# Kernel optimization log

Hardware: AMD Instinct MI355X
Metric: run time of the kernel (lower is better)

Reference implementation:

```python
import jax, jax.numpy as jnp
import numpy as np

N_EMBD = 1024
N_HEAD = 16
HEAD_DIM = N_EMBD // N_HEAD


def setup_inputs() -> dict:
    key = jax.random.key(0)
    ks = jax.random.split(key, 5)
    scale = 0.02
    x = jax.random.normal(ks[0], (2, 2048, N_EMBD), dtype=jnp.float32)
    w_attn = jax.random.normal(ks[1], (N_EMBD, 3 * N_EMBD), dtype=jnp.float32) * scale
    b_attn = jax.random.normal(ks[2], (3 * N_EMBD,), dtype=jnp.float32) * scale
    w_proj = jax.random.normal(ks[3], (N_EMBD, N_EMBD), dtype=jnp.float32) * scale
    b_proj = jax.random.normal(ks[4], (N_EMBD,), dtype=jnp.float32) * scale
    return {"x": x, "w_attn": w_attn, "b_attn": b_attn, "w_proj": w_proj, "b_proj": b_proj}


def reference(x, w_attn, b_attn, w_proj, b_proj):
    B, T, C = x.shape
    qkv = x @ w_attn + b_attn  # [B,T,3C]
    q, k, v = jnp.split(qkv, 3, axis=-1)
    # [B, H, T, D]
    q = q.reshape(B, T, N_HEAD, HEAD_DIM).transpose(0, 2, 1, 3)
    k = k.reshape(B, T, N_HEAD, HEAD_DIM).transpose(0, 2, 1, 3)
    v = v.reshape(B, T, N_HEAD, HEAD_DIM).transpose(0, 2, 1, 3)
    att = jnp.einsum("bhqd,bhkd->bhqk", q, k) * (1.0 / np.sqrt(HEAD_DIM))
    causal = jnp.tril(jnp.ones((T, T), dtype=bool))
    att = jnp.where(causal[None, None], att, jnp.float32(-jnp.inf))
    att = jax.nn.softmax(att, axis=-1)
    y = jnp.einsum("bhqk,bhkd->bhqd", att, v)  # [B,H,T,D]
    y = y.transpose(0, 2, 1, 3).reshape(B, T, C)
    return y @ w_proj + b_proj
```

## Files before the change

### kernel.cpp

```cpp
#include <hip/hip_runtime.h>
#include <stdint.h>

#define SEQ   2048
#define EMBD  1024
#define M_ROWS 4096

typedef unsigned short u16;
typedef unsigned int u32;
typedef __attribute__((ext_vector_type(8))) short bf16x8;
typedef __attribute__((ext_vector_type(4))) float f32x4;

__device__ __forceinline__ u16 f2b(float f) {
  u32 x = __float_as_uint(f);
  return (u16)((x + 0x7FFFu + ((x >> 16) & 1u)) >> 16);
}

__device__ __forceinline__ u32 pkbf(float a, float b) {
  u32 r;
  asm("v_cvt_pk_bf16_f32 %0, %1, %2" : "=v"(r) : "v"(a), "v"(b));
  return r;
}

__device__ __forceinline__ float exp2fast(float x) {
#if __has_builtin(__builtin_amdgcn_exp2f)
  return __builtin_amdgcn_exp2f(x);
#else
  return __expf(x * 0.69314718f);
#endif
}

__device__ __forceinline__ float rcpfast(float x) {
#if __has_builtin(__builtin_amdgcn_rcpf)
  return __builtin_amdgcn_rcpf(x);
#else
  return 1.f / x;
#endif
}

#define AS1(p) ((const __attribute__((address_space(1))) void*)(uintptr_t)(p))
#define AS3(p) ((__attribute__((address_space(3))) void*)(uintptr_t)(p))

__global__ __launch_bounds__(256) void prep(
    const float* __restrict__ x, u16* __restrict__ xb,
    const float* __restrict__ wa, u16* __restrict__ wat,
    const float* __restrict__ wp, u16* __restrict__ wpt) {
  __shared__ float t[64][65];
  const int bx = blockIdx.x;
  if (bx < 1024) {
    const size_t idx = (size_t)bx * 256 + threadIdx.x;
    const float4* p = (const float4*)x + 4 * idx;
    uint4 o0, o1;
    {
      float4 a = p[0], b = p[1];
      o0.x = (u32)f2b(a.x) | ((u32)f2b(a.y) << 16);
      o0.y = (u32)f2b(a.z) | ((u32)f2b(a.w) << 16);
      o0.z = (u32)f2b(b.x) | ((u32)f2b(b.y) << 16);
      o0.w = (u32)f2b(b.z) | ((u32)f2b(b.w) << 16);
    }
    {
      float4 a = p[2], b = p[3];
      o1.x = (u32)f2b(a.x) | ((u32)f2b(a.y) << 16);
      o1.y = (u32)f2b(a.z) | ((u32)f2b(a.w) << 16);
      o1.z = (u32)f2b(b.x) | ((u32)f2b(b.y) << 16);
      o1.w = (u32)f2b(b.z) | ((u32)f2b(b.w) << 16);
    }
    ((uint4*)xb)[2 * idx] = o0;
    ((uint4*)xb)[2 * idx + 1] = o1;
    return;
  }
  const int tt = bx - 1024;
  const int bxr = tt & 63, by = tt >> 6;
  const float* w = (bxr < 48) ? wa : wp;
  u16* wt = (bxr < 48) ? wat : wpt;
  const int N = (bxr < 48) ? 3072 : 1024;
  const int bxt = (bxr < 48) ? bxr : bxr - 48;
  const int K = 1024;
  const int n0 = bxt * 64, k0 = by * 64;
  const int c = threadIdx.x & 63, r4 = threadIdx.x >> 6;
#pragma unroll
  for (int j = 0; j < 16; ++j) {
    const int r = j * 4 + r4;
    t[c][r] = w[(size_t)(k0 + r) * N + n0 + c];
  }
  __syncthreads();
#pragma unroll
  for (int j = 0; j < 16; ++j) {
    const int nr = j * 4 + r4;
    wt[(size_t)(n0 + nr) * K + k0 + c] = f2b(t[nr][c]);
  }
}

template <bool OUT_BF16>
__global__ __launch_bounds__(256) void gemm_kmajor(
    const u16* __restrict__ A, const u16* __restrict__ Bt,
    const float* __restrict__ bias, void* __restrict__ outp,
    int M, int N, int K, int nbx) {
  __shared__ __align__(16) u16 sm[2][2][128 * 32];

  const int nwg = gridDim.x;
  const int qq = nwg >> 3, rr = nwg & 7;
  const int xcd = blockIdx.x & 7, off = blockIdx.x >> 3;
  const int wgid = (xcd < rr ? xcd * (qq + 1) : rr * (qq + 1) + (xcd - rr) * qq) + off;
  const int bx = wgid % nbx, by = wgid / nbx;
  const int row0 = by * 128, col0 = bx * 128;

  const int tid = threadIdx.x;
  const int w = tid >> 6, lane = tid & 63;
  const int wrow = (w >> 1) * 64, wcol = (w & 1) * 64;

  f32x4 acc[4][4];
#pragma unroll
  for (int a = 0; a < 4; ++a)
#pragma unroll
    for (int b = 0; b < 4; ++b)
#pragma unroll
      for (int e = 0; e < 4; ++e) acc[a][b][e] = 0.f;

  const size_t Kb = (size_t)K * 2;

  auto stage = [&](int k0, int buf) {
#pragma unroll
    for (int c = 0; c < 4; ++c) {
      const int ch = w * 4 + c;
      const int i = ch & 7;
      const int rloc = i * 16 + (lane >> 2);
      const int kb = ((lane & 3) * 16) ^ ((rloc & 3) << 4);
      const u16* mat = (ch < 8) ? A : Bt;
      const int r0 = (ch < 8) ? row0 : col0;
      const char* src = (const char*)mat + (size_t)(r0 + rloc) * Kb + k0 * 2 + kb;
      char* dst = (char*)&sm[buf][(ch < 8) ? 0 : 1][0] + i * 1024;
      __builtin_amdgcn_global_load_lds(AS1(src), AS3(dst), 16, 0, 0);
    }
  };

  auto compute = [&](int buf) {
    bf16x8 af[4], bfr[4];
    const char* As = (const char*)&sm[buf][0][0];
    const char* Bs = (const char*)&sm[buf][1][0];
#pragma unroll
    for (int rb = 0; rb < 4; ++rb) {
      const int rl = wrow + rb * 16 + (lane & 15);
      const int kb2 = ((lane >> 4) * 16) ^ ((rl & 3) << 4);
      af[rb] = *(const bf16x8*)(As + rl * 64 + kb2);
    }
#pragma unroll
    for (int cb = 0; cb < 4; ++cb) {
      const int rl = wcol + cb * 16 + (lane & 15);
      const int kb2 = ((lane >> 4) * 16) ^ ((rl & 3) << 4);
      bfr[cb] = *(const bf16x8*)(Bs + rl * 64 + kb2);
    }
#pragma unroll
    for (int rb = 0; rb < 4; ++rb)
#pragma unroll
      for (int cb = 0; cb < 4; ++cb)
        acc[rb][cb] = __builtin_amdgcn_mfma_f32_16x16x32_bf16(
            af[rb], bfr[cb], acc[rb][cb], 0, 0, 0);
  };

  const int nt = K >> 5;
  stage(0, 0);
  int cur = 0;
  for (int t = 0; t < nt - 1; ++t) {
    __syncthreads();
    stage((t + 1) * 32, cur ^ 1);
    compute(cur);
    cur ^= 1;
  }
  __syncthreads();
  compute(cur);

#pragma unroll
  for (int cb = 0; cb < 4; ++cb) {
    const int colg = col0 + wcol + cb * 16 + (lane & 15);
    const float bv = bias[colg];
#pragma unroll
    for (int rb = 0; rb < 4; ++rb) {
#pragma unroll
      for (int i = 0; i < 4; ++i) {
        const int rowg = row0 + wrow + rb * 16 + (lane >> 4) * 4 + i;
        const float v = acc[rb][cb][i] + bv;
        if (OUT_BF16) {
          const u32 hv = f2b(v);
          const u32 pv = (u32)__shfl_xor((int)hv, 1);
          if (!(lane & 1))
            *(u32*)((u16*)outp + (size_t)rowg * N + colg) = hv | (pv << 16);
        } else {
          ((float*)outp)[(size_t)rowg * N + colg] = v;
        }
      }
    }
  }
}

__global__ __launch_bounds__(256, 4) void attn_mfma2(
    const u16* __restrict__ qkvb, u16* __restrict__ yb) {
  __shared__ __align__(16) char lds[32768];

  const int bx = blockIdx.x;
  const int xcd = bx & 7, g = bx >> 3;
  const int j = g >> 5, r = g & 31;
  const int bh = xcd * 4 + j;
  const int qt = (j & 1) ? r : 31 - r;
  const int bb = bh >> 4, h = bh & 15;

  const int tid = threadIdx.x;
  const int w = tid >> 6, lane = tid & 63;
  const int hh = lane >> 4, qh = lane & 15;

  const size_t rowb = 6144;
  const char* base = (const char*)qkvb + (size_t)bb * SEQ * rowb;
  const int koffb = EMBD * 2 + h * 128;
  const int voffb = 2 * EMBD * 2 + h * 128;

  const int krow_in_chunk = lane >> 3;
  const int vkv = (tid & 31) * 2;
  const int vdg = tid >> 5;

  const int q_abs = qt * 64 + w * 16 + qh;
  const int qloc = w * 16 + qh;

  const char* qp = base + (size_t)q_abs * rowb + h * 128 + hh * 16;
  const bf16x8 qf0 = *(const bf16x8*)qp;
  const bf16x8 qf1 = *(const bf16x8*)(qp + 64);

  float m2 = -1e30f, l = 0.f;
  f32x4 of[4];
#pragma unroll
  for (int db = 0; db < 4; ++db)
#pragma unroll
    for (int e = 0; e < 4; ++e) of[db][e] = 0.f;

  {
#pragma unroll
    for (int cc = 0; cc < 2; ++cc) {
      const int i = w * 2 + cc;
      const int kvl = i * 8 + krow_in_chunk;
      const int gs = (lane & 7) ^ ((i & 3) | ((krow_in_chunk & 1) << 2));
      const char* src = base + (size_t)kvl * rowb + koffb + gs * 16;
      __builtin_amdgcn_global_load_lds(AS1(src), AS3(lds + i * 1024), 16, 0, 0);
    }
    const char* vp = base + (size_t)vkv * rowb + voffb + vdg * 16;
    uint4 va = *(const uint4*)vp;
    uint4 vb = *(const uint4*)(vp + rowb);
    union { uint4 q; u16 s[8]; } ua, ub;
    ua.q = va; ub.q = vb;
    u32* vt = (u32*)(lds + 16384);
#pragma unroll
    for (int e = 0; e < 8; ++e) {
      const int d = vdg * 8 + e;
      vt[d * 32 + ((vkv >> 1) ^ ((d & 7) << 2))] =
          (u32)ua.s[e] | ((u32)ub.s[e] << 16);
    }
  }
  __syncthreads();

  for (int kt = 0; kt <= qt; ++kt) {
    const int cur = kt & 1;
    const char* ksb = lds + cur * 8192;
    const char* vtb = lds + 16384 + cur * 8192;

    uint4 va, vb;
    const bool pref = (kt < qt);
    if (pref) {
#pragma unroll
      for (int cc = 0; cc < 2; ++cc) {
        const int i = w * 2 + cc;
        const int kvl = i * 8 + krow_in_chunk;
        const int gs = (lane & 7) ^ ((i & 3) | ((krow_in_chunk & 1) << 2));
        const char* src =
            base + (size_t)((kt + 1) * 64 + kvl) * rowb + koffb + gs * 16;
        __builtin_amdgcn_global_load_lds(
            AS1(src), AS3(lds + (cur ^ 1) * 8192 + i * 1024), 16, 0, 0);
      }
      const char* vp =
          base + (size_t)((kt + 1) * 64 + vkv) * rowb + voffb + vdg * 16;
      va = *(const uint4*)vp;
      vb = *(const uint4*)(vp + rowb);
    }

    f32x4 st[4];
    __builtin_amdgcn_s_setprio(1);
#pragma unroll
    for (int rb = 0; rb < 4; ++rb) {
#pragma unroll
      for (int e = 0; e < 4; ++e) st[rb][e] = 0.f;
      const int kv = 32 * (rb >> 1) + 8 * ((lane >> 2) & 3) + 4 * (rb & 1) +
                     (lane & 3);
      const int f = ((kv >> 3) & 3) | ((kv & 1) << 2);
      const char* rp = ksb + kv * 128;
      const bf16x8 k0 = *(const bf16x8*)(rp + ((hh * 16) ^ (f << 4)));
      const bf16x8 k1 = *(const bf16x8*)(rp + ((64 + hh * 16) ^ (f << 4)));
      st[rb] = __builtin_amdgcn_mfma_f32_16x16x32_bf16(k0, qf0, st[rb], 0, 0, 0);
      st[rb] = __builtin_amdgcn_mfma_f32_16x16x32_bf16(k1, qf1, st[rb], 0, 0, 0);
    }
    __builtin_amdgcn_s_setprio(0);

    const float C = 0.18033688f;
    float pmax = -3.0e38f;
    if (kt == qt) {
#pragma unroll
      for (int rb = 0; rb < 4; ++rb) {
        const int kvb = 32 * (rb >> 1) + 8 * hh + 4 * (rb & 1);
#pragma unroll
        for (int i = 0; i < 4; ++i) {
          float v = st[rb][i] * C;
          if (kvb + i > qloc) v = -3.0e38f;
          st[rb][i] = v;
          pmax = fmaxf(pmax, v);
        }
      }
    } else {
#pragma unroll
      for (int rb = 0; rb < 4; ++rb)
#pragma unroll
        for (int i = 0; i < 4; ++i) {
          const float v = st[rb][i] * C;
          st[rb][i] = v;
          pmax = fmaxf(pmax, v);
        }
    }
    pmax = fmaxf(pmax, __shfl_xor(pmax, 16));
    pmax = fmaxf(pmax, __shfl_xor(pmax, 32));

    if (__any(pmax > m2 + 5.f)) {
      const float mn = fmaxf(m2, pmax);
      const float al = exp2fast(m2 - mn);
      m2 = mn;
      l *= al;
#pragma unroll
      for (int db = 0; db < 4; ++db)
#pragma unroll
        for (int e = 0; e < 4; ++e) of[db][e] *= al;
    }

    float ls = 0.f;
#pragma unroll
    for (int rb = 0; rb < 4; ++rb)
#pragma unroll
      for (int i = 0; i < 4; ++i) {
        const float p = exp2fast(st[rb][i] - m2);
        st[rb][i] = p;
        ls += p;
      }
    ls += __shfl_xor(ls, 16);
    ls += __shfl_xor(ls, 32);
    l += ls;

    union { u32 wd[4]; bf16x8 v; } pf0, pf1;
    pf0.wd[0] = pkbf(st[0][0], st[0][1]);
    pf0.wd[1] = pkbf(st[0][2], st[0][3]);
    pf0.wd[2] = pkbf(st[1][0], st[1][1]);
    pf0.wd[3] = pkbf(st[1][2], st[1][3]);
    pf1.wd[0] = pkbf(st[2][0], st[2][1]);
    pf1.wd[1] = pkbf(st[2][2], st[2][3]);
    pf1.wd[2] = pkbf(st[3][0], st[3][1]);
    pf1.wd[3] = pkbf(st[3][2], st[3][3]);

    __builtin_amdgcn_s_setprio(1);
#pragma unroll
    for (int db = 0; db < 4; ++db) {
      const int d = db * 16 + qh;
      const int g2 = d & 7;
      const char* rp = vtb + d * 128;
      const bf16x8 v0 = *(const bf16x8*)(rp + ((hh * 16) ^ (g2 << 4)));
      const bf16x8 v1 = *(const bf16x8*)(rp + ((64 + hh * 16) ^ (g2 << 4)));
      of[db] = __builtin_amdgcn_mfma_f32_16x16x32_bf16(v0, pf0.v, of[db], 0, 0, 0);
      of[db] = __builtin_amdgcn_mfma_f32_16x16x32_bf16(v1, pf1.v, of[db], 0, 0, 0);
    }
    __builtin_amdgcn_s_setprio(0);

    if (pref) {
      union { uint4 q; u16 s[8]; } ua, ub;
      ua.q = va; ub.q = vb;
      u32* vt = (u32*)(lds + 16384 + (cur ^ 1) * 8192);
#pragma unroll
      for (int e = 0; e < 8; ++e) {
        const int d = vdg * 8 + e;
        vt[d * 32 + ((vkv >> 1) ^ ((d & 7) << 2))] =
            (u32)ua.s[e] | ((u32)ub.s[e] << 16);
      }
    }
    __syncthreads();
  }

  const float inv = rcpfast(l);
  u16* yrow = yb + (size_t)(bb * SEQ + q_abs) * EMBD + h * 64;
#pragma unroll
  for (int db = 0; db < 4; ++db) {
    const u32 w0 = pkbf(of[db][0] * inv, of[db][1] * inv);
    const u32 w1 = pkbf(of[db][2] * inv, of[db][3] * inv);
    *(u32*)(yrow + db * 16 + 4 * hh) = w0;
    *(u32*)(yrow + db * 16 + 4 * hh + 2) = w1;
  }
}

extern "C" void kernel_launch(void* const* d_in, const int* in_sizes, int n_in,
                              void* d_out, int out_size, void* d_ws,
                              size_t ws_size, hipStream_t stream) {
  const float* x      = (const float*)d_in[0];
  const float* w_attn = (const float*)d_in[1];
  const float* b_attn = (const float*)d_in[2];
  const float* w_proj = (const float*)d_in[3];
  const float* b_proj = (const float*)d_in[4];
  float* out = (float*)d_out;

  u16* xb   = (u16*)d_ws;
  u16* wat  = xb + (size_t)M_ROWS * EMBD;
  u16* wpt  = wat + (size_t)3 * EMBD * EMBD;
  u16* qkvb = wpt + (size_t)EMBD * EMBD;
  u16* yb   = qkvb + (size_t)M_ROWS * 3 * EMBD;

  prep<<<2048, 256, 0, stream>>>(x, xb, w_attn, wat, w_proj, wpt);

  gemm_kmajor<true><<<768, 256, 0, stream>>>(
      xb, wat, b_attn, qkvb, M_ROWS, 3 * EMBD, EMBD, 24);

  attn_mfma2<<<1024, 256, 0, stream>>>(qkvb, yb);

  gemm_kmajor<false><<<256, 256, 0, stream>>>(
      yb, wpt, b_proj, out, M_ROWS, EMBD, EMBD, 8);
}
```

Baseline: 184.5 us.

## Triple-buffer GEMM and attention loads, pair causal q-tiles, fold softmax scale into QKV

```diff
diff --git a/kernel.cpp b/kernel.cpp
--- a/kernel.cpp
+++ b/kernel.cpp
@@ -39,6 +39,9 @@
 
 #define AS1(p) ((const __attribute__((address_space(1))) void*)(uintptr_t)(p))
 #define AS3(p) ((__attribute__((address_space(3))) void*)(uintptr_t)(p))
+#define VMCNT(n) asm volatile("s_waitcnt vmcnt(" #n ")" ::: "memory")
+#define LGKM0    asm volatile("s_waitcnt lgkmcnt(0)" ::: "memory")
+#define SCHED0   __builtin_amdgcn_sched_barrier(0)
 
 __global__ __launch_bounds__(256) void prep(
     const float* __restrict__ x, u16* __restrict__ xb,
@@ -90,12 +93,12 @@
   }
 }
 
-template <bool OUT_BF16>
+template <bool OUT_BF16, bool SCALEQ>
 __global__ __launch_bounds__(256) void gemm_kmajor(
     const u16* __restrict__ A, const u16* __restrict__ Bt,
     const float* __restrict__ bias, void* __restrict__ outp,
     int M, int N, int K, int nbx) {
-  __shared__ __align__(16) u16 sm[2][2][128 * 32];
+  __shared__ __align__(16) u16 sm[3][2][128 * 32];
 
   const int nwg = gridDim.x;
   const int qq = nwg >> 3, rr = nwg & 7;
@@ -159,26 +162,38 @@
 
   const int nt = K >> 5;
   stage(0, 0);
-  int cur = 0;
-  for (int t = 0; t < nt - 1; ++t) {
-    __syncthreads();
-    stage((t + 1) * 32, cur ^ 1);
-    compute(cur);
-    cur ^= 1;
-  }
-  __syncthreads();
-  compute(cur);
-
+  SCHED0;
+  stage(32, 1);
+  SCHED0;
+  VMCNT(4);
+  SCHED0;
+  __builtin_amdgcn_s_barrier();
+
+  int bc = 0, bn = 1, bnn = 2;
+  for (int t = 0; t < nt; ++t) {
+    if (t + 2 < nt) stage((t + 2) * 32, bnn);
+    compute(bc);
+    if (t + 1 < nt) {
+      if (t + 2 < nt) { VMCNT(4); } else { VMCNT(0); }
+      SCHED0;
+      __builtin_amdgcn_s_barrier();
+    }
+    const int tmp = bc; bc = bn; bn = bnn; bnn = tmp;
+  }
+
+  const float C = 0.18033688f;
 #pragma unroll
   for (int cb = 0; cb < 4; ++cb) {
     const int colg = col0 + wcol + cb * 16 + (lane & 15);
     const float bv = bias[colg];
+    const bool doscale = SCALEQ && (colg < 1024);
 #pragma unroll
     for (int rb = 0; rb < 4; ++rb) {
 #pragma unroll
       for (int i = 0; i < 4; ++i) {
         const int rowg = row0 + wrow + rb * 16 + (lane >> 4) * 4 + i;
-        const float v = acc[rb][cb][i] + bv;
+        float v = acc[rb][cb][i] + bv;
+        if (doscale) v *= C;
         if (OUT_BF16) {
           const u32 hv = f2b(v);
           const u32 pv = (u32)__shfl_xor((int)hv, 1);
@@ -192,15 +207,13 @@
   }
 }
 
-__global__ __launch_bounds__(256, 4) void attn_mfma2(
+__global__ __launch_bounds__(256, 2) void attn_mfma3(
     const u16* __restrict__ qkvb, u16* __restrict__ yb) {
-  __shared__ __align__(16) char lds[32768];
+  __shared__ __align__(16) char lds[49152];
 
   const int bx = blockIdx.x;
-  const int xcd = bx & 7, g = bx >> 3;
-  const int j = g >> 5, r = g & 31;
-  const int bh = xcd * 4 + j;
-  const int qt = (j & 1) ? r : 31 - r;
+  const int pr = bx >> 5;
+  const int bh = bx & 31;
   const int bb = bh >> 4, h = bh & 15;
 
   const int tid = threadIdx.x;
@@ -216,181 +229,185 @@
   const int vkv = (tid & 31) * 2;
   const int vdg = tid >> 5;
 
-  const int q_abs = qt * 64 + w * 16 + qh;
-  const int qloc = w * 16 + qh;
-
-  const char* qp = base + (size_t)q_abs * rowb + h * 128 + hh * 16;
-  const bf16x8 qf0 = *(const bf16x8*)qp;
-  const bf16x8 qf1 = *(const bf16x8*)(qp + 64);
-
-  float m2 = -1e30f, l = 0.f;
-  f32x4 of[4];
-#pragma unroll
-  for (int db = 0; db < 4; ++db)
-#pragma unroll
-    for (int e = 0; e < 4; ++e) of[db][e] = 0.f;
-
-  {
-#pragma unroll
-    for (int cc = 0; cc < 2; ++cc) {
-      const int i = w * 2 + cc;
-      const int kvl = i * 8 + krow_in_chunk;
-      const int gs = (lane & 7) ^ ((i & 3) | ((krow_in_chunk & 1) << 2));
-      const char* src = base + (size_t)kvl * rowb + koffb + gs * 16;
-      __builtin_amdgcn_global_load_lds(AS1(src), AS3(lds + i * 1024), 16, 0, 0);
-    }
-    const char* vp = base + (size_t)vkv * rowb + voffb + vdg * 16;
-    uint4 va = *(const uint4*)vp;
-    uint4 vb = *(const uint4*)(vp + rowb);
-    union { uint4 q; u16 s[8]; } ua, ub;
-    ua.q = va; ub.q = vb;
-    u32* vt = (u32*)(lds + 16384);
-#pragma unroll
-    for (int e = 0; e < 8; ++e) {
-      const int d = vdg * 8 + e;
-      vt[d * 32 + ((vkv >> 1) ^ ((d & 7) << 2))] =
-          (u32)ua.s[e] | ((u32)ub.s[e] << 16);
-    }
-  }
-  __syncthreads();
-
-  for (int kt = 0; kt <= qt; ++kt) {
-    const int cur = kt & 1;
-    const char* ksb = lds + cur * 8192;
-    const char* vtb = lds + 16384 + cur * 8192;
-
-    uint4 va, vb;
-    const bool pref = (kt < qt);
-    if (pref) {
+  for (int half = 0; half < 2; ++half) {
+    const int qt = half ? pr : 31 - pr;
+    const int q_abs = qt * 64 + w * 16 + qh;
+    const int qloc = w * 16 + qh;
+
+    const char* qp = base + (size_t)q_abs * rowb + h * 128 + hh * 16;
+    const bf16x8 qf0 = *(const bf16x8*)qp;
+    const bf16x8 qf1 = *(const bf16x8*)(qp + 64);
+    SCHED0;
+
+    float m2 = -1e30f, l = 0.f;
+    f32x4 of[4];
+#pragma unroll
+    for (int db = 0; db < 4; ++db)
+#pragma unroll
+      for (int e = 0; e < 4; ++e) of[db][e] = 0.f;
+
+    auto issueV = [&](int kt, uint4& a, uint4& b) {
+      const char* vp = base + (size_t)(kt * 64 + vkv) * rowb + voffb + vdg * 16;
+      a = *(const uint4*)vp;
+      b = *(const uint4*)(vp + rowb);
+    };
+    auto issueK = [&](int kt, int buf) {
 #pragma unroll
       for (int cc = 0; cc < 2; ++cc) {
         const int i = w * 2 + cc;
         const int kvl = i * 8 + krow_in_chunk;
         const int gs = (lane & 7) ^ ((i & 3) | ((krow_in_chunk & 1) << 2));
-        const char* src =
-            base + (size_t)((kt + 1) * 64 + kvl) * rowb + koffb + gs * 16;
-        __builtin_amdgcn_global_load_lds(
-            AS1(src), AS3(lds + (cur ^ 1) * 8192 + i * 1024), 16, 0, 0);
-      }
-      const char* vp =
-          base + (size_t)((kt + 1) * 64 + vkv) * rowb + voffb + vdg * 16;
-      va = *(const uint4*)vp;
-      vb = *(const uint4*)(vp + rowb);
-    }
-
-    f32x4 st[4];
-    __builtin_amdgcn_s_setprio(1);
-#pragma unroll
-    for (int rb = 0; rb < 4; ++rb) {
-#pragma unroll
-      for (int e = 0; e < 4; ++e) st[rb][e] = 0.f;
-      const int kv = 32 * (rb >> 1) + 8 * ((lane >> 2) & 3) + 4 * (rb & 1) +
-                     (lane & 3);
-      const int f = ((kv >> 3) & 3) | ((kv & 1) << 2);
-      const char* rp = ksb + kv * 128;
-      const bf16x8 k0 = *(const bf16x8*)(rp + ((hh * 16) ^ (f << 4)));
-      const bf16x8 k1 = *(const bf16x8*)(rp + ((64 + hh * 16) ^ (f << 4)));
-      st[rb] = __builtin_amdgcn_mfma_f32_16x16x32_bf16(k0, qf0, st[rb], 0, 0, 0);
-      st[rb] = __builtin_amdgcn_mfma_f32_16x16x32_bf16(k1, qf1, st[rb], 0, 0, 0);
-    }
-    __builtin_amdgcn_s_setprio(0);
-
-    const float C = 0.18033688f;
-    float pmax = -3.0e38f;
-    if (kt == qt) {
-#pragma unroll
-      for (int rb = 0; rb < 4; ++rb) {
-        const int kvb = 32 * (rb >> 1) + 8 * hh + 4 * (rb & 1);
-#pragma unroll
-        for (int i = 0; i < 4; ++i) {
-          float v = st[rb][i] * C;
-          if (kvb + i > qloc) v = -3.0e38f;
-          st[rb][i] = v;
-          pmax = fmaxf(pmax, v);
-        }
-      }
-    } else {
-#pragma unroll
-      for (int rb = 0; rb < 4; ++rb)
-#pragma unroll
-        for (int i = 0; i < 4; ++i) {
-          const float v = st[rb][i] * C;
-          st[rb][i] = v;
-          pmax = fmaxf(pmax, v);
-        }
-    }
-    pmax = fmaxf(pmax, __shfl_xor(pmax, 16));
-    pmax = fmaxf(pmax, __shfl_xor(pmax, 32));
-
-    if (__any(pmax > m2 + 5.f)) {
-      const float mn = fmaxf(m2, pmax);
-      const float al = exp2fast(m2 - mn);
-      m2 = mn;
-      l *= al;
-#pragma unroll
-      for (int db = 0; db < 4; ++db)
-#pragma unroll
-        for (int e = 0; e < 4; ++e) of[db][e] *= al;
-    }
-
-    float ls = 0.f;
-#pragma unroll
-    for (int rb = 0; rb < 4; ++rb)
-#pragma unroll
-      for (int i = 0; i < 4; ++i) {
-        const float p = exp2fast(st[rb][i] - m2);
-        st[rb][i] = p;
-        ls += p;
-      }
-    ls += __shfl_xor(ls, 16);
-    ls += __shfl_xor(ls, 32);
-    l += ls;
-
-    union { u32 wd[4]; bf16x8 v; } pf0, pf1;
-    pf0.wd[0] = pkbf(st[0][0], st[0][1]);
-    pf0.wd[1] = pkbf(st[0][2], st[0][3]);
-    pf0.wd[2] = pkbf(st[1][0], st[1][1]);
-    pf0.wd[3] = pkbf(st[1][2], st[1][3]);
-    pf1.wd[0] = pkbf(st[2][0], st[2][1]);
-    pf1.wd[1] = pkbf(st[2][2], st[2][3]);
-    pf1.wd[2] = pkbf(st[3][0], st[3][1]);
-    pf1.wd[3] = pkbf(st[3][2], st[3][3]);
-
-    __builtin_amdgcn_s_setprio(1);
-#pragma unroll
-    for (int db = 0; db < 4; ++db) {
-      const int d = db * 16 + qh;
-      const int g2 = d & 7;
-      const char* rp = vtb + d * 128;
-      const bf16x8 v0 = *(const bf16x8*)(rp + ((hh * 16) ^ (g2 << 4)));
-      const bf16x8 v1 = *(const bf16x8*)(rp + ((64 + hh * 16) ^ (g2 << 4)));
-      of[db] = __builtin_amdgcn_mfma_f32_16x16x32_bf16(v0, pf0.v, of[db], 0, 0, 0);
-      of[db] = __builtin_amdgcn_mfma_f32_16x16x32_bf16(v1, pf1.v, of[db], 0, 0, 0);
-    }
-    __builtin_amdgcn_s_setprio(0);
-
-    if (pref) {
+        const char* src = base + (size_t)(kt * 64 + kvl) * rowb + koffb + gs * 16;
+        __builtin_amdgcn_global_load_lds(AS1(src),
+                                         AS3(lds + buf * 8192 + i * 1024), 16, 0, 0);
+      }
+    };
+    auto writeV = [&](const uint4& a, const uint4& b, int buf) {
       union { uint4 q; u16 s[8]; } ua, ub;
-      ua.q = va; ub.q = vb;
-      u32* vt = (u32*)(lds + 16384 + (cur ^ 1) * 8192);
+      ua.q = a; ub.q = b;
+      u32* vt = (u32*)(lds + 24576 + buf * 8192);
 #pragma unroll
       for (int e = 0; e < 8; ++e) {
         const int d = vdg * 8 + e;
         vt[d * 32 + ((vkv >> 1) ^ ((d & 7) << 2))] =
             (u32)ua.s[e] | ((u32)ub.s[e] << 16);
       }
+    };
+
+    uint4 v0a, v0b, vpa, vpb, vna = {}, vnb = {};
+    issueV(0, v0a, v0b);
+    SCHED0;
+    issueK(0, 0);
+    SCHED0;
+    issueV(1, vpa, vpb);
+    SCHED0;
+    issueK(1, 1);
+    SCHED0;
+    VMCNT(6);
+    SCHED0;
+    writeV(v0a, v0b, 0);
+    VMCNT(4);
+    LGKM0;
+    SCHED0;
+    __builtin_amdgcn_s_barrier();
+
+    int bc = 0, bn = 1, bnn = 2;
+    for (int kt = 0; kt <= qt; ++kt) {
+      const char* ksb = lds + bc * 8192;
+      const char* vtb = lds + 24576 + bc * 8192;
+
+      const bool pref2 = (kt + 2 <= qt);
+      if (pref2) {
+        issueV(kt + 2, vna, vnb);
+        issueK(kt + 2, bnn);
+      }
+
+      f32x4 st[4];
+      __builtin_amdgcn_s_setprio(1);
+#pragma unroll
+      for (int rb = 0; rb < 4; ++rb) {
+#pragma unroll
+        for (int e = 0; e < 4; ++e) st[rb][e] = 0.f;
+        const int kv = 32 * (rb >> 1) + 8 * ((lane >> 2) & 3) + 4 * (rb & 1) +
+                       (lane & 3);
+        const int f = ((kv >> 3) & 3) | ((kv & 1) << 2);
+        const char* rp = ksb + kv * 128;
+        const bf16x8 k0 = *(const bf16x8*)(rp + ((hh * 16) ^ (f << 4)));
+        const bf16x8 k1 = *(const bf16x8*)(rp + ((64 + hh * 16) ^ (f << 4)));
+        st[rb] = __builtin_amdgcn_mfma_f32_16x16x32_bf16(k0, qf0, st[rb], 0, 0, 0);
+        st[rb] = __builtin_amdgcn_mfma_f32_16x16x32_bf16(k1, qf1, st[rb], 0, 0, 0);
+      }
+      __builtin_amdgcn_s_setprio(0);
+
+      float pmax = -3.0e38f;
+      if (kt == qt) {
+#pragma unroll
+        for (int rb = 0; rb < 4; ++rb) {
+          const int kvb = 32 * (rb >> 1) + 8 * hh + 4 * (rb & 1);
+#pragma unroll
+          for (int i = 0; i < 4; ++i) {
+            float v = st[rb][i];
+            if (kvb + i > qloc) v = -3.0e38f;
+            st[rb][i] = v;
+            pmax = fmaxf(pmax, v);
+          }
+        }
+      } else {
+#pragma unroll
+        for (int rb = 0; rb < 4; ++rb)
+#pragma unroll
+          for (int i = 0; i < 4; ++i) pmax = fmaxf(pmax, st[rb][i]);
+      }
+      pmax = fmaxf(pmax, __shfl_xor(pmax, 16));
+      pmax = fmaxf(pmax, __shfl_xor(pmax, 32));
+
+      if (__any(pmax > m2 + 5.f)) {
+        const float mn = fmaxf(m2, pmax);
+        const float al = exp2fast(m2 - mn);
+        m2 = mn;
+        l *= al;
+#pragma unroll
+        for (int db = 0; db < 4; ++db)
+#pragma unroll
+          for (int e = 0; e < 4; ++e) of[db][e] *= al;
+      }
+
+#pragma unroll
+      for (int rb = 0; rb < 4; ++rb)
+#pragma unroll
+        for (int i = 0; i < 4; ++i) {
+          const float p = exp2fast(st[rb][i] - m2);
+          st[rb][i] = p;
+          l += p;
+        }
+
+      union { u32 wd[4]; bf16x8 v; } pf0, pf1;
+      pf0.wd[0] = pkbf(st[0][0], st[0][1]);
+      pf0.wd[1] = pkbf(st[0][2], st[0][3]);
+      pf0.wd[2] = pkbf(st[1][0], st[1][1]);
+      pf0.wd[3] = pkbf(st[1][2], st[1][3]);
+      pf1.wd[0] = pkbf(st[2][0], st[2][1]);
+      pf1.wd[1] = pkbf(st[2][2], st[2][3]);
+      pf1.wd[2] = pkbf(st[3][0], st[3][1]);
+      pf1.wd[3] = pkbf(st[3][2], st[3][3]);
+
+      __builtin_amdgcn_s_setprio(1);
+#pragma unroll
+      for (int db = 0; db < 4; ++db) {
+        const int d = db * 16 + qh;
+        const int g2 = d & 7;
+        const char* rp = vtb + d * 128;
+        const bf16x8 v0 = *(const bf16x8*)(rp + ((hh * 16) ^ (g2 << 4)));
+        const bf16x8 v1 = *(const bf16x8*)(rp + ((64 + hh * 16) ^ (g2 << 4)));
+        of[db] = __builtin_amdgcn_mfma_f32_16x16x32_bf16(v0, pf0.v, of[db], 0, 0, 0);
+        of[db] = __builtin_amdgcn_mfma_f32_16x16x32_bf16(v1, pf1.v, of[db], 0, 0, 0);
+      }
+      __builtin_amdgcn_s_setprio(0);
+
+      if (kt < qt) {
+        if (pref2) { VMCNT(4); } else { VMCNT(0); }
+        SCHED0;
+        writeV(vpa, vpb, bn);
+        LGKM0;
+        SCHED0;
+        __builtin_amdgcn_s_barrier();
+        vpa = vna; vpb = vnb;
+      }
+      const int tmp = bc; bc = bn; bn = bnn; bnn = tmp;
+    }
+
+    l += __shfl_xor(l, 16);
+    l += __shfl_xor(l, 32);
+    const float inv = rcpfast(l);
+    u16* yrow = yb + (size_t)(bb * SEQ + q_abs) * EMBD + h * 64;
+#pragma unroll
+    for (int db = 0; db < 4; ++db) {
+      const u32 w0 = pkbf(of[db][0] * inv, of[db][1] * inv);
+      const u32 w1 = pkbf(of[db][2] * inv, of[db][3] * inv);
+      *(u32*)(yrow + db * 16 + 4 * hh) = w0;
+      *(u32*)(yrow + db * 16 + 4 * hh + 2) = w1;
     }
     __syncthreads();
-  }
-
-  const float inv = rcpfast(l);
-  u16* yrow = yb + (size_t)(bb * SEQ + q_abs) * EMBD + h * 64;
-#pragma unroll
-  for (int db = 0; db < 4; ++db) {
-    const u32 w0 = pkbf(of[db][0] * inv, of[db][1] * inv);
-    const u32 w1 = pkbf(of[db][2] * inv, of[db][3] * inv);
-    *(u32*)(yrow + db * 16 + 4 * hh) = w0;
-    *(u32*)(yrow + db * 16 + 4 * hh + 2) = w1;
   }
 }
 
@@ -412,11 +429,11 @@
 
   prep<<<2048, 256, 0, stream>>>(x, xb, w_attn, wat, w_proj, wpt);
 
-  gemm_kmajor<true><<<768, 256, 0, stream>>>(
+  gemm_kmajor<true, true><<<768, 256, 0, stream>>>(
       xb, wat, b_attn, qkvb, M_ROWS, 3 * EMBD, EMBD, 24);
 
-  attn_mfma2<<<1024, 256, 0, stream>>>(qkvb, yb);
-
-  gemm_kmajor<false><<<256, 256, 0, stream>>>(
+  attn_mfma3<<<512, 256, 0, stream>>>(qkvb, yb);
+
+  gemm_kmajor<false, false><<<256, 256, 0, stream>>>(
       yb, wpt, b_proj, out, M_ROWS, EMBD, EMBD, 8);
 }
```

Measured after the change: 185.0 us. Within noise of the previous version (+0.3%).

## Triple-buffer GEMM loads, fold softmax scale into QKV epilogue, defer row-sum reduction

Applied to the files above, without the earlier changes.

```diff
diff --git a/kernel.cpp b/kernel.cpp
--- a/kernel.cpp
+++ b/kernel.cpp
@@ -39,6 +39,9 @@
 
 #define AS1(p) ((const __attribute__((address_space(1))) void*)(uintptr_t)(p))
 #define AS3(p) ((__attribute__((address_space(3))) void*)(uintptr_t)(p))
+#define VMCNT(n) asm volatile("s_waitcnt vmcnt(" #n ")" ::: "memory")
+#define LGKM0    asm volatile("s_waitcnt lgkmcnt(0)" ::: "memory")
+#define SCHED0   __builtin_amdgcn_sched_barrier(0)
 
 __global__ __launch_bounds__(256) void prep(
     const float* __restrict__ x, u16* __restrict__ xb,
@@ -90,12 +93,12 @@
   }
 }
 
-template <bool OUT_BF16>
+template <bool OUT_BF16, bool SCALEQ>
 __global__ __launch_bounds__(256) void gemm_kmajor(
     const u16* __restrict__ A, const u16* __restrict__ Bt,
     const float* __restrict__ bias, void* __restrict__ outp,
     int M, int N, int K, int nbx) {
-  __shared__ __align__(16) u16 sm[2][2][128 * 32];
+  __shared__ __align__(16) u16 sm[3][2][128 * 32];
 
   const int nwg = gridDim.x;
   const int qq = nwg >> 3, rr = nwg & 7;
@@ -149,36 +152,50 @@
       const int kb2 = ((lane >> 4) * 16) ^ ((rl & 3) << 4);
       bfr[cb] = *(const bf16x8*)(Bs + rl * 64 + kb2);
     }
+    __builtin_amdgcn_s_setprio(1);
 #pragma unroll
     for (int rb = 0; rb < 4; ++rb)
 #pragma unroll
       for (int cb = 0; cb < 4; ++cb)
         acc[rb][cb] = __builtin_amdgcn_mfma_f32_16x16x32_bf16(
             af[rb], bfr[cb], acc[rb][cb], 0, 0, 0);
+    __builtin_amdgcn_s_setprio(0);
   };
 
   const int nt = K >> 5;
   stage(0, 0);
-  int cur = 0;
-  for (int t = 0; t < nt - 1; ++t) {
-    __syncthreads();
-    stage((t + 1) * 32, cur ^ 1);
-    compute(cur);
-    cur ^= 1;
-  }
-  __syncthreads();
-  compute(cur);
-
+  SCHED0;
+  stage(32, 1);
+  SCHED0;
+  VMCNT(4);
+  SCHED0;
+  __builtin_amdgcn_s_barrier();
+
+  int bc = 0, bn = 1, bnn = 2;
+  for (int t = 0; t < nt; ++t) {
+    if (t + 2 < nt) stage((t + 2) * 32, bnn);
+    compute(bc);
+    if (t + 1 < nt) {
+      if (t + 2 < nt) { VMCNT(4); } else { VMCNT(0); }
+      SCHED0;
+      __builtin_amdgcn_s_barrier();
+    }
+    const int tmp = bc; bc = bn; bn = bnn; bnn = tmp;
+  }
+
+  const float C = 0.18033688f;
 #pragma unroll
   for (int cb = 0; cb < 4; ++cb) {
     const int colg = col0 + wcol + cb * 16 + (lane & 15);
     const float bv = bias[colg];
+    const bool doscale = SCALEQ && (colg < 1024);
 #pragma unroll
     for (int rb = 0; rb < 4; ++rb) {
 #pragma unroll
       for (int i = 0; i < 4; ++i) {
         const int rowg = row0 + wrow + rb * 16 + (lane >> 4) * 4 + i;
-        const float v = acc[rb][cb][i] + bv;
+        float v = acc[rb][cb][i] + bv;
+        if (doscale) v *= C;
         if (OUT_BF16) {
           const u32 hv = f2b(v);
           const u32 pv = (u32)__shfl_xor((int)hv, 1);
@@ -295,7 +312,6 @@
     }
     __builtin_amdgcn_s_setprio(0);
 
-    const float C = 0.18033688f;
     float pmax = -3.0e38f;
     if (kt == qt) {
 #pragma unroll
@@ -303,21 +319,15 @@
         const int kvb = 32 * (rb >> 1) + 8 * hh + 4 * (rb & 1);
 #pragma unroll
         for (int i = 0; i < 4; ++i) {
-          float v = st[rb][i] * C;
-          if (kvb + i > qloc) v = -3.0e38f;
-          st[rb][i] = v;
-          pmax = fmaxf(pmax, v);
+          if (kvb + i > qloc) st[rb][i] = -3.0e38f;
+          pmax = fmaxf(pmax, st[rb][i]);
         }
       }
     } else {
 #pragma unroll
       for (int rb = 0; rb < 4; ++rb)
 #pragma unroll
-        for (int i = 0; i < 4; ++i) {
-          const float v = st[rb][i] * C;
-          st[rb][i] = v;
-          pmax = fmaxf(pmax, v);
-        }
+        for (int i = 0; i < 4; ++i) pmax = fmaxf(pmax, st[rb][i]);
     }
     pmax = fmaxf(pmax, __shfl_xor(pmax, 16));
     pmax = fmaxf(pmax, __shfl_xor(pmax, 32));
@@ -333,18 +343,14 @@
         for (int e = 0; e < 4; ++e) of[db][e] *= al;
     }
 
-    float ls = 0.f;
 #pragma unroll
     for (int rb = 0; rb < 4; ++rb)
 #pragma unroll
       for (int i = 0; i < 4; ++i) {
         const float p = exp2fast(st[rb][i] - m2);
         st[rb][i] = p;
-        ls += p;
+        l += p;
       }
-    ls += __shfl_xor(ls, 16);
-    ls += __shfl_xor(ls, 32);
-    l += ls;
 
     union { u32 wd[4]; bf16x8 v; } pf0, pf1;
     pf0.wd[0] = pkbf(st[0][0], st[0][1]);
@@ -383,6 +389,8 @@
     __syncthreads();
   }
 
+  l += __shfl_xor(l, 16);
+  l += __shfl_xor(l, 32);
   const float inv = rcpfast(l);
   u16* yrow = yb + (size_t)(bb * SEQ + q_abs) * EMBD + h * 64;
 #pragma unroll
@@ -412,11 +420,11 @@
 
   prep<<<2048, 256, 0, stream>>>(x, xb, w_attn, wat, w_proj, wpt);
 
-  gemm_kmajor<true><<<768, 256, 0, stream>>>(
+  gemm_kmajor<true, true><<<768, 256, 0, stream>>>(
       xb, wat, b_attn, qkvb, M_ROWS, 3 * EMBD, EMBD, 24);
 
   attn_mfma2<<<1024, 256, 0, stream>>>(qkvb, yb);
 
-  gemm_kmajor<false><<<256, 256, 0, stream>>>(
+  gemm_kmajor<false, false><<<256, 256, 0, stream>>>(
       yb, wpt, b_proj, out, M_ROWS, EMBD, EMBD, 8);
 }
```

Measured after the change: 183.0 us. About the same (-0.8%).
